# Kernel optimization log

Measured on AMD Instinct MI355X. Metric: run time of the kernel, lower is better.

Reference implementation:

```python
import jax, jax.numpy as jnp
import numpy as np

T = 16777216            # flat replay-buffer length (timesteps)
DISCOUNT = 0.99         # gamma
FINAL_REWARD = 0.0      # bootstrap value for the last timestep
TERM_PROB = 0.001       # ~1000-step episodes


def setup_inputs() -> dict:
    key = jax.random.key(0)
    k1, k2 = jax.random.split(key)
    reward = jax.random.normal(k1, (T,), dtype=jnp.float32)
    terminal = jax.random.bernoulli(k2, TERM_PROB, (T,))
    return {"terminal": terminal, "reward": reward}


def _discounted_cumret(terminal, reward):
    # Reverse-time linear recurrence (same math as tf.scan over reversed seq):
    #   c_t = r_t                      if terminal_t
    #   c_t = r_t + discount * c_{t+1} otherwise
    # i.e. c_t = a_t * c_{t+1} + b_t with a_t = discount*(1-term_t), b_t = r_t.
    # Expressed as a (log-depth) associative scan over the reversed sequence.
    a = jnp.where(terminal, jnp.zeros((), reward.dtype),
                  jnp.asarray(DISCOUNT, reward.dtype))
    a_rev = a[::-1]
    b_rev = reward[::-1]
    # fold the initializer (final_reward) into the first reversed element
    b_rev = b_rev.at[0].add(a_rev[0] * jnp.asarray(FINAL_REWARD, reward.dtype))

    def combine(e1, e2):
        # composition of affine maps x -> a*x + b (e1 applied first)
        a1, b1 = e1
        a2, b2 = e2
        return a1 * a2, a2 * b1 + b2

    _, y_rev = jax.lax.associative_scan(combine, (a_rev, b_rev))
    return y_rev[::-1]


def reference(terminal, reward):
    return _discounted_cumret(terminal, reward)
```

## Files before the change

kernel.cpp:

```cpp
#include <hip/hip_runtime.h>


constexpr int   TPB   = 256;
constexpr int   IPTC  = 8;
constexpr int   NCH   = 4;
constexpr int   CHUNK = TPB * IPTC;
constexpr int   TILE  = CHUNK * NCH;
constexpr float DISC  = 0.99f;
constexpr float L2DISC = -0.0144995696f;

__device__ __forceinline__ void wave_suffix_scan(float& A, float& B, int lane) {
    #pragma unroll
    for (int off = 1; off < 64; off <<= 1) {
        float oA = __shfl_down(A, off, 64);
        float oB = __shfl_down(B, off, 64);
        if (lane + off < 64) { B = A * oB + B; A = A * oA; }
    }
}

__global__ __launch_bounds__(TPB) void k_local(
        const int* __restrict__ term, const float* __restrict__ rew,
        float* __restrict__ out, float2* __restrict__ agg,
        int* __restrict__ lastT, long long T) {
    __shared__ float2 sWA[TPB / 64];
    __shared__ int    sLast[TPB / 64];

    const int t = threadIdx.x;
    const int lane = t & 63, wav = t >> 6;
    const int b = blockIdx.x;
    const long long lo = (long long)b * TILE;
    const bool fastblk = (lo + TILE <= T);

    float At = 1.f, Bt = 0.f;
    int   lt = -1;

    if (fastblk) {
        float4 bR[2][IPTC / 4];
        int4   bT[2][IPTC / 4];

        {
            const long long base = lo + (long long)(NCH - 1) * CHUNK
                                      + (long long)t * IPTC;
            const float4* rp = (const float4*)(rew + base);
            const int4*   tp = (const int4*)(term + base);
            #pragma unroll
            for (int q = 0; q < IPTC / 4; ++q) {
                bR[(NCH - 1) & 1][q] = rp[q];
                bT[(NCH - 1) & 1][q] = tp[q];
            }
        }

        #pragma unroll
        for (int c = NCH - 1; c >= 0; --c) {
            if (c > 0) {
                const long long nbase = lo + (long long)(c - 1) * CHUNK
                                           + (long long)t * IPTC;
                const float4* rp = (const float4*)(rew + nbase);
                const int4*   tp = (const int4*)(term + nbase);
                #pragma unroll
                for (int q = 0; q < IPTC / 4; ++q) {
                    bR[(c - 1) & 1][q] = rp[q];
                    bT[(c - 1) & 1][q] = tp[q];
                }
            }
            const int p = c & 1;
            const long long base = lo + (long long)c * CHUNK + (long long)t * IPTC;

            float r[IPTC];
            unsigned mask = 0;
            #pragma unroll
            for (int q = 0; q < IPTC / 4; ++q) {
                float4 rv = bR[p][q];
                int4   tv = bT[p][q];
                r[4*q+0] = rv.x; r[4*q+1] = rv.y; r[4*q+2] = rv.z; r[4*q+3] = rv.w;
                mask |= (tv.x ? 1u : 0u) << (4*q+0);
                mask |= (tv.y ? 1u : 0u) << (4*q+1);
                mask |= (tv.z ? 1u : 0u) << (4*q+2);
                mask |= (tv.w ? 1u : 0u) << (4*q+3);
            }

            float A = 1.f, B = 0.f;
            #pragma unroll
            for (int k = IPTC - 1; k >= 0; --k) {
                float ak = ((mask >> k) & 1u) ? 0.f : DISC;
                B = ak * B + r[k]; A = ak * A;
            }

            float IA = A, IB = B;
            wave_suffix_scan(IA, IB, lane);

            int myLast = mask ? (int)(base + (31 - __clz(mask))) : -1;
            #pragma unroll
            for (int off = 32; off > 0; off >>= 1)
                myLast = max(myLast, __shfl_down(myLast, off, 64));

            if (lane == 0) { sWA[wav] = make_float2(IA, IB); sLast[wav] = myLast; }
            __syncthreads();

            float2 g = sWA[0];
            int cl = sLast[0];
            #pragma unroll
            for (int w = 1; w < TPB / 64; ++w) {
                float2 h = sWA[w];
                g.y = g.x * h.y + g.y; g.x = g.x * h.x;
                cl = max(cl, sLast[w]);
            }
            float EWA = 1.f, EWB = 0.f;
            #pragma unroll
            for (int w = 0; w < TPB / 64; ++w)
                if (w > wav) { float2 h = sWA[w]; EWB = EWA*h.y + EWB; EWA = EWA*h.x; }

            float EA = __shfl_down(IA, 1, 64);
            float EB = __shfl_down(IB, 1, 64);
            if (lane == 63) { EA = 1.f; EB = 0.f; }

            const float Yc = Bt;
            float y = EA * (EWA * Yc + EWB) + EB;

            #pragma unroll
            for (int k = IPTC - 1; k >= 0; --k) {
                float ak = ((mask >> k) & 1u) ? 0.f : DISC;
                y = ak * y + r[k]; r[k] = y;
            }

            float4* op = (float4*)(out + base);
            #pragma unroll
            for (int q = 0; q < IPTC / 4; ++q)
                op[q] = make_float4(r[4*q+0], r[4*q+1], r[4*q+2], r[4*q+3]);

            Bt = g.x * Bt + g.y;
            At = g.x * At;
            lt = max(lt, cl);
            __syncthreads();
        }
    } else {
        for (int c = NCH - 1; c >= 0; --c) {
            const long long base = lo + (long long)c * CHUNK + (long long)t * IPTC;
            float r[IPTC];
            unsigned mask = 0;
            #pragma unroll
            for (int k = 0; k < IPTC; ++k) {
                long long i = base + k;
                if (i < T) { r[k] = rew[i]; mask |= (term[i] ? 1u : 0u) << k; }
                else       { r[k] = 0.f; }
            }
            float A = 1.f, B = 0.f;
            #pragma unroll
            for (int k = IPTC - 1; k >= 0; --k) {
                float ak = ((mask >> k) & 1u) ? 0.f : DISC;
                if (base + k >= T) ak = 1.f;
                B = ak * B + r[k]; A = ak * A;
            }
            float IA = A, IB = B;
            wave_suffix_scan(IA, IB, lane);

            int myLast = mask ? (int)(base + (31 - __clz(mask))) : -1;
            #pragma unroll
            for (int off = 32; off > 0; off >>= 1)
                myLast = max(myLast, __shfl_down(myLast, off, 64));

            if (lane == 0) { sWA[wav] = make_float2(IA, IB); sLast[wav] = myLast; }
            __syncthreads();

            float2 g = sWA[0];
            int cl = sLast[0];
            #pragma unroll
            for (int w = 1; w < TPB / 64; ++w) {
                float2 h = sWA[w];
                g.y = g.x * h.y + g.y; g.x = g.x * h.x;
                cl = max(cl, sLast[w]);
            }
            float EWA = 1.f, EWB = 0.f;
            #pragma unroll
            for (int w = 0; w < TPB / 64; ++w)
                if (w > wav) { float2 h = sWA[w]; EWB = EWA*h.y + EWB; EWA = EWA*h.x; }

            float EA = __shfl_down(IA, 1, 64);
            float EB = __shfl_down(IB, 1, 64);
            if (lane == 63) { EA = 1.f; EB = 0.f; }

            const float Yc = Bt;
            float y = EA * (EWA * Yc + EWB) + EB;

            #pragma unroll
            for (int k = IPTC - 1; k >= 0; --k) {
                float ak = ((mask >> k) & 1u) ? 0.f : DISC;
                if (base + k >= T) ak = 1.f;
                y = ak * y + r[k]; r[k] = y;
            }
            #pragma unroll
            for (int k = 0; k < IPTC; ++k) {
                long long i = base + k;
                if (i < T) out[i] = r[k];
            }

            Bt = g.x * Bt + g.y;
            At = g.x * At;
            lt = max(lt, cl);
            __syncthreads();
        }
    }

    if (t == 0) {
        agg[b] = make_float2(At, Bt);
        lastT[b] = max(lt, (int)lo - 1);
    }
}

__global__ __launch_bounds__(TPB) void k_fix(
        const float2* __restrict__ agg, const int* __restrict__ lastT,
        float* __restrict__ out, int numBlocks, long long T) {
    __shared__ float2 sWB[TPB / 64];

    const int t = threadIdx.x;
    const int lane = t & 63, wav = t >> 6;
    const int b = blockIdx.x;

    const int cpt = (numBlocks + TPB - 1) / TPB;
    float VA = 1.f, VB = 0.f;
    #pragma unroll
    for (int k = cpt - 1; k >= 0; --k) {
        int g = t * cpt + k;
        if (g > b && g < numBlocks) {
            float2 q = agg[g];
            VB = q.x * VB + q.y; VA = q.x * VA;
        }
    }
    wave_suffix_scan(VA, VB, lane);
    if (lane == 0) sWB[wav] = make_float2(VA, VB);
    __syncthreads();

    float FA = sWB[0].x, FB = sWB[0].y;
    #pragma unroll
    for (int w = 1; w < TPB / 64; ++w) {
        float2 h = sWB[w];
        FB = FA * h.y + FB; FA = FA * h.x;
    }
    const float yin = FB;
    if (yin == 0.f) return;

    const long long lo = (long long)b * TILE;
    const long long hi = min(lo + TILE, T) - 1;
    const long long start = (long long)lastT[b] + 1;

    for (long long i = start + t; i <= hi; i += TPB) {
        float d = (float)(int)(hi + 1 - i);
        out[i] += exp2f(d * L2DISC) * yin;
    }
}

extern "C" void kernel_launch(void* const* d_in, const int* in_sizes, int n_in,
                              void* d_out, int out_size, void* d_ws, size_t ws_size,
                              hipStream_t stream) {
    const int*   term = (const int*)d_in[0];
    const float* rew  = (const float*)d_in[1];
    float*       out  = (float*)d_out;

    const long long T = (long long)in_sizes[1];
    const int numBlocks = (int)((T + TILE - 1) / TILE);

    float2* agg   = (float2*)d_ws;
    int*    lastT = (int*)(agg + numBlocks);

    k_local<<<numBlocks, TPB, 0, stream>>>(term, rew, out, agg, lastT, T);
    k_fix  <<<numBlocks, TPB, 0, stream>>>(agg, lastT, out, numBlocks, T);
}
```

Before: 179.4 us.

## Fuse two-pass scan into single-pass decoupled look-back kernel

Replaces the separate local-scan and fix-up kernels with one kernel. Blocks take dynamic tile indices from an atomic ticket (processed from the end of the sequence) and publish per-tile aggregates and inclusive values through flags, using a wave-wide decoupled look-back to obtain the incoming carry. This removes the second launch and the global re-read of aggregates. Output stores also become nontemporal. It adds a memset, atomics and spin-waiting, and the fix-up pass now read-modify-writes output that was just stored with nontemporal hints.

```diff
diff --git a/kernel.cpp b/kernel.cpp
--- a/kernel.cpp
+++ b/kernel.cpp
@@ -9,6 +9,10 @@
 constexpr float DISC  = 0.99f;
 constexpr float L2DISC = -0.0144995696f;
 
+#define SCOPE_AGENT __HIP_MEMORY_SCOPE_AGENT
+
+typedef float vf4 __attribute__((ext_vector_type(4)));
+
 __device__ __forceinline__ void wave_suffix_scan(float& A, float& B, int lane) {
     #pragma unroll
     for (int off = 1; off < 64; off <<= 1) {
@@ -18,16 +22,24 @@
     }
 }
 
-__global__ __launch_bounds__(TPB) void k_local(
+__global__ __launch_bounds__(TPB) void k_scan(
         const int* __restrict__ term, const float* __restrict__ rew,
-        float* __restrict__ out, float2* __restrict__ agg,
-        int* __restrict__ lastT, long long T) {
+        float* __restrict__ out,
+        int* __restrict__ flags, int* __restrict__ ticket,
+        unsigned long long* __restrict__ AB, float* __restrict__ Incl,
+        int nB, long long T) {
     __shared__ float2 sWA[TPB / 64];
     __shared__ int    sLast[TPB / 64];
+    __shared__ int    sVb;
+    __shared__ float  sYin;
 
     const int t = threadIdx.x;
     const int lane = t & 63, wav = t >> 6;
-    const int b = blockIdx.x;
+
+    if (t == 0) sVb = atomicAdd(ticket, 1);
+    __syncthreads();
+    const int vb = sVb;
+    const int b  = nB - 1 - vb;
     const long long lo = (long long)b * TILE;
     const bool fastblk = (lo + TILE <= T);
 
@@ -123,10 +135,12 @@
                 y = ak * y + r[k]; r[k] = y;
             }
 
-            float4* op = (float4*)(out + base);
-            #pragma unroll
-            for (int q = 0; q < IPTC / 4; ++q)
-                op[q] = make_float4(r[4*q+0], r[4*q+1], r[4*q+2], r[4*q+3]);
+            vf4* op = (vf4*)(out + base);
+            #pragma unroll
+            for (int q = 0; q < IPTC / 4; ++q) {
+                vf4 v = { r[4*q+0], r[4*q+1], r[4*q+2], r[4*q+3] };
+                __builtin_nontemporal_store(v, op + q);
+            }
 
             Bt = g.x * Bt + g.y;
             At = g.x * At;
@@ -202,50 +216,79 @@
     }
 
     if (t == 0) {
-        agg[b] = make_float2(At, Bt);
-        lastT[b] = max(lt, (int)lo - 1);
-    }
-}
-
-__global__ __launch_bounds__(TPB) void k_fix(
-        const float2* __restrict__ agg, const int* __restrict__ lastT,
-        float* __restrict__ out, int numBlocks, long long T) {
-    __shared__ float2 sWB[TPB / 64];
-
-    const int t = threadIdx.x;
-    const int lane = t & 63, wav = t >> 6;
-    const int b = blockIdx.x;
-
-    const int cpt = (numBlocks + TPB - 1) / TPB;
-    float VA = 1.f, VB = 0.f;
-    #pragma unroll
-    for (int k = cpt - 1; k >= 0; --k) {
-        int g = t * cpt + k;
-        if (g > b && g < numBlocks) {
-            float2 q = agg[g];
-            VB = q.x * VB + q.y; VA = q.x * VA;
-        }
-    }
-    wave_suffix_scan(VA, VB, lane);
-    if (lane == 0) sWB[wav] = make_float2(VA, VB);
+        union { float2 f; unsigned long long u; } c;
+        c.f = make_float2(At, Bt);
+        __hip_atomic_store(&AB[vb], c.u, __ATOMIC_RELAXED, SCOPE_AGENT);
+        __hip_atomic_store(&flags[vb], 1, __ATOMIC_RELEASE, SCOPE_AGENT);
+    }
+
+    if (wav == 0) {
+        float yin = 0.f;
+        float Ca = 1.f, Cb = 0.f;
+        int look = vb - 1;
+        for (;;) {
+            if (look < 0 || Ca == 0.f) { yin = Cb; break; }
+            const int p = look - lane;
+            int f = 0;
+            if (p >= 0) f = __hip_atomic_load(&flags[p], __ATOMIC_ACQUIRE, SCOPE_AGENT);
+            const unsigned long long balP = __ballot(f == 2);
+            const unsigned long long balA = __ballot(f != 0);
+            const unsigned long long vmask =
+                (look >= 63) ? ~0ull : ((1ull << (look + 1)) - 1ull);
+            const unsigned long long prefAvail = balP & vmask;
+            bool consumed = false;
+            if (prefAvail) {
+                const int lp = (int)__ffsll((long long)prefAvail) - 1;
+                const unsigned long long need = (1ull << lp) - 1ull;
+                if ((balA & need) == need) {
+                    float a = 1.f, bv = 0.f;
+                    if (lane < lp) {
+                        union { unsigned long long u; float2 f2; } c;
+                        c.u = __hip_atomic_load(&AB[p], __ATOMIC_RELAXED, SCOPE_AGENT);
+                        a = c.f2.x; bv = c.f2.y;
+                    } else if (lane == lp) {
+                        a = 0.f;
+                        bv = __hip_atomic_load(&Incl[p], __ATOMIC_RELAXED, SCOPE_AGENT);
+                    }
+                    wave_suffix_scan(a, bv, lane);
+                    bv = __shfl(bv, 0, 64);
+                    yin = Ca * bv + Cb;
+                    break;
+                }
+            }
+            if ((balA & vmask) == vmask) {
+                float a = 1.f, bv = 0.f;
+                if (p >= 0) {
+                    union { unsigned long long u; float2 f2; } c;
+                    c.u = __hip_atomic_load(&AB[p], __ATOMIC_RELAXED, SCOPE_AGENT);
+                    a = c.f2.x; bv = c.f2.y;
+                }
+                wave_suffix_scan(a, bv, lane);
+                const float wA = __shfl(a, 0, 64);
+                const float wB = __shfl(bv, 0, 64);
+                Cb = Ca * wB + Cb;
+                Ca = Ca * wA;
+                look -= 64;
+                consumed = true;
+            }
+            if (!consumed) __builtin_amdgcn_s_sleep(2);
+        }
+        if (lane == 0) {
+            sYin = yin;
+            __hip_atomic_store(&Incl[vb], At * yin + Bt, __ATOMIC_RELAXED, SCOPE_AGENT);
+            __hip_atomic_store(&flags[vb], 2, __ATOMIC_RELEASE, SCOPE_AGENT);
+        }
+    }
     __syncthreads();
-
-    float FA = sWB[0].x, FB = sWB[0].y;
-    #pragma unroll
-    for (int w = 1; w < TPB / 64; ++w) {
-        float2 h = sWB[w];
-        FB = FA * h.y + FB; FA = FA * h.x;
-    }
-    const float yin = FB;
-    if (yin == 0.f) return;
-
-    const long long lo = (long long)b * TILE;
-    const long long hi = min(lo + TILE, T) - 1;
-    const long long start = (long long)lastT[b] + 1;
-
-    for (long long i = start + t; i <= hi; i += TPB) {
-        float d = (float)(int)(hi + 1 - i);
-        out[i] += exp2f(d * L2DISC) * yin;
+    const float yin = sYin;
+
+    if (yin != 0.f) {
+        const long long hi = min(lo + (long long)TILE, T) - 1;
+        const long long start = (long long)max(lt, (int)lo - 1) + 1;
+        for (long long i = start + t; i <= hi; i += TPB) {
+            float d = (float)(int)(hi + 1 - i);
+            out[i] += exp2f(d * L2DISC) * yin;
+        }
     }
 }
 
@@ -257,11 +300,14 @@
     float*       out  = (float*)d_out;
 
     const long long T = (long long)in_sizes[1];
-    const int numBlocks = (int)((T + TILE - 1) / TILE);
-
-    float2* agg   = (float2*)d_ws;
-    int*    lastT = (int*)(agg + numBlocks);
-
-    k_local<<<numBlocks, TPB, 0, stream>>>(term, rew, out, agg, lastT, T);
-    k_fix  <<<numBlocks, TPB, 0, stream>>>(agg, lastT, out, numBlocks, T);
+    const int nB = (int)((T + TILE - 1) / TILE);
+
+    int* flags  = (int*)d_ws;
+    int* ticket = flags + nB;
+    size_t off = (((size_t)(nB + 1) * 4) + 15) & ~(size_t)15;
+    unsigned long long* AB = (unsigned long long*)((char*)d_ws + off);
+    float* Incl = (float*)(AB + nB);
+
+    (void)hipMemsetAsync(d_ws, 0, (size_t)(nB + 1) * 4, stream);
+    k_scan<<<nB, TPB, 0, stream>>>(term, rew, out, flags, ticket, AB, Incl, nB, T);
 }
```

After: 468.1 us. 2.61x slower.

## Preload all chunks up front and double-buffer shared aggregates to drop barrier

Applied to the files above, without the earlier changes.

Issues every chunk's reward and terminal loads for the tile at kernel start instead of prefetching one chunk ahead. This raises memory-level parallelism. Per-wave scan aggregates in shared memory are double-buffered by chunk parity, so the trailing __syncthreads per chunk can be removed. The cost is more live registers for the load buffers, which may lower occupancy.

```diff
diff --git a/kernel.cpp b/kernel.cpp
--- a/kernel.cpp
+++ b/kernel.cpp
@@ -22,8 +22,8 @@
         const int* __restrict__ term, const float* __restrict__ rew,
         float* __restrict__ out, float2* __restrict__ agg,
         int* __restrict__ lastT, long long T) {
-    __shared__ float2 sWA[TPB / 64];
-    __shared__ int    sLast[TPB / 64];
+    __shared__ float2 sWA[2][TPB / 64];
+    __shared__ int    sLast[2][TPB / 64];
 
     const int t = threadIdx.x;
     const int lane = t & 63, wav = t >> 6;
@@ -35,43 +35,32 @@
     int   lt = -1;
 
     if (fastblk) {
-        float4 bR[2][IPTC / 4];
-        int4   bT[2][IPTC / 4];
-
-        {
-            const long long base = lo + (long long)(NCH - 1) * CHUNK
-                                      + (long long)t * IPTC;
+        float4 bR[NCH][IPTC / 4];
+        int4   bT[NCH][IPTC / 4];
+
+        #pragma unroll
+        for (int c = NCH - 1; c >= 0; --c) {
+            const long long base = lo + (long long)c * CHUNK + (long long)t * IPTC;
             const float4* rp = (const float4*)(rew + base);
             const int4*   tp = (const int4*)(term + base);
             #pragma unroll
             for (int q = 0; q < IPTC / 4; ++q) {
-                bR[(NCH - 1) & 1][q] = rp[q];
-                bT[(NCH - 1) & 1][q] = tp[q];
+                bR[c][q] = rp[q];
+                bT[c][q] = tp[q];
             }
         }
 
         #pragma unroll
         for (int c = NCH - 1; c >= 0; --c) {
-            if (c > 0) {
-                const long long nbase = lo + (long long)(c - 1) * CHUNK
-                                           + (long long)t * IPTC;
-                const float4* rp = (const float4*)(rew + nbase);
-                const int4*   tp = (const int4*)(term + nbase);
-                #pragma unroll
-                for (int q = 0; q < IPTC / 4; ++q) {
-                    bR[(c - 1) & 1][q] = rp[q];
-                    bT[(c - 1) & 1][q] = tp[q];
-                }
-            }
-            const int p = c & 1;
+            const int pb = c & 1;
             const long long base = lo + (long long)c * CHUNK + (long long)t * IPTC;
 
             float r[IPTC];
             unsigned mask = 0;
             #pragma unroll
             for (int q = 0; q < IPTC / 4; ++q) {
-                float4 rv = bR[p][q];
-                int4   tv = bT[p][q];
+                float4 rv = bR[c][q];
+                int4   tv = bT[c][q];
                 r[4*q+0] = rv.x; r[4*q+1] = rv.y; r[4*q+2] = rv.z; r[4*q+3] = rv.w;
                 mask |= (tv.x ? 1u : 0u) << (4*q+0);
                 mask |= (tv.y ? 1u : 0u) << (4*q+1);
@@ -94,21 +83,21 @@
             for (int off = 32; off > 0; off >>= 1)
                 myLast = max(myLast, __shfl_down(myLast, off, 64));
 
-            if (lane == 0) { sWA[wav] = make_float2(IA, IB); sLast[wav] = myLast; }
+            if (lane == 0) { sWA[pb][wav] = make_float2(IA, IB); sLast[pb][wav] = myLast; }
             __syncthreads();
 
-            float2 g = sWA[0];
-            int cl = sLast[0];
+            float2 g = sWA[pb][0];
+            int cl = sLast[pb][0];
             #pragma unroll
             for (int w = 1; w < TPB / 64; ++w) {
-                float2 h = sWA[w];
+                float2 h = sWA[pb][w];
                 g.y = g.x * h.y + g.y; g.x = g.x * h.x;
-                cl = max(cl, sLast[w]);
+                cl = max(cl, sLast[pb][w]);
             }
             float EWA = 1.f, EWB = 0.f;
             #pragma unroll
             for (int w = 0; w < TPB / 64; ++w)
-                if (w > wav) { float2 h = sWA[w]; EWB = EWA*h.y + EWB; EWA = EWA*h.x; }
+                if (w > wav) { float2 h = sWA[pb][w]; EWB = EWA*h.y + EWB; EWA = EWA*h.x; }
 
             float EA = __shfl_down(IA, 1, 64);
             float EB = __shfl_down(IB, 1, 64);
@@ -131,10 +120,10 @@
             Bt = g.x * Bt + g.y;
             At = g.x * At;
             lt = max(lt, cl);
-            __syncthreads();
         }
     } else {
         for (int c = NCH - 1; c >= 0; --c) {
+            const int pb = c & 1;
             const long long base = lo + (long long)c * CHUNK + (long long)t * IPTC;
             float r[IPTC];
             unsigned mask = 0;
@@ -159,21 +148,21 @@
             for (int off = 32; off > 0; off >>= 1)
                 myLast = max(myLast, __shfl_down(myLast, off, 64));
 
-            if (lane == 0) { sWA[wav] = make_float2(IA, IB); sLast[wav] = myLast; }
+            if (lane == 0) { sWA[pb][wav] = make_float2(IA, IB); sLast[pb][wav] = myLast; }
             __syncthreads();
 
-            float2 g = sWA[0];
-            int cl = sLast[0];
+            float2 g = sWA[pb][0];
+            int cl = sLast[pb][0];
             #pragma unroll
             for (int w = 1; w < TPB / 64; ++w) {
-                float2 h = sWA[w];
+                float2 h = sWA[pb][w];
                 g.y = g.x * h.y + g.y; g.x = g.x * h.x;
-                cl = max(cl, sLast[w]);
+                cl = max(cl, sLast[pb][w]);
             }
             float EWA = 1.f, EWB = 0.f;
             #pragma unroll
             for (int w = 0; w < TPB / 64; ++w)
-                if (w > wav) { float2 h = sWA[w]; EWB = EWA*h.y + EWB; EWA = EWA*h.x; }
+                if (w > wav) { float2 h = sWA[pb][w]; EWB = EWA*h.y + EWB; EWA = EWA*h.x; }
 
             float EA = __shfl_down(IA, 1, 64);
             float EB = __shfl_down(IB, 1, 64);
@@ -197,7 +186,6 @@
             Bt = g.x * Bt + g.y;
             At = g.x * At;
             lt = max(lt, cl);
-            __syncthreads();
         }
     }
 
```

Result: no change. 178.3 us (-0.6%).

## Replace per-block chunk loop with single 1024-thread tile per block

Applied to the files above, without the earlier changes.

The local scan kernel now uses 1024-thread blocks that each process one 8192-element tile in a single pass, replacing 256-thread blocks that looped over four chunks with double-buffered prefetch and carried state between them. This removes the serial chunk loop, the carry propagation and a barrier per chunk. The fix kernel keeps 256 threads via a separate constant. Tiles are the same size, so block counts are unchanged. The cost is that the within-block cross-wave combine now spans 16 waves serially, and the explicit load prefetch is gone.

```diff
diff --git a/kernel.cpp b/kernel.cpp
--- a/kernel.cpp
+++ b/kernel.cpp
@@ -1,13 +1,14 @@
 #include <hip/hip_runtime.h>
 
 
-constexpr int   TPB   = 256;
+constexpr int   TPB   = 1024;
+constexpr int   NWAV  = TPB / 64;
 constexpr int   IPTC  = 8;
-constexpr int   NCH   = 4;
-constexpr int   CHUNK = TPB * IPTC;
-constexpr int   TILE  = CHUNK * NCH;
+constexpr int   TILE  = TPB * IPTC;
 constexpr float DISC  = 0.99f;
 constexpr float L2DISC = -0.0144995696f;
+
+constexpr int   FTPB  = 256;
 
 __device__ __forceinline__ void wave_suffix_scan(float& A, float& B, int lane) {
     #pragma unroll
@@ -22,8 +23,8 @@
         const int* __restrict__ term, const float* __restrict__ rew,
         float* __restrict__ out, float2* __restrict__ agg,
         int* __restrict__ lastT, long long T) {
-    __shared__ float2 sWA[TPB / 64];
-    __shared__ int    sLast[TPB / 64];
+    __shared__ float2 sWA[NWAV];
+    __shared__ int    sLast[NWAV];
 
     const int t = threadIdx.x;
     const int lane = t & 63, wav = t >> 6;
@@ -31,174 +32,146 @@
     const long long lo = (long long)b * TILE;
     const bool fastblk = (lo + TILE <= T);
 
-    float At = 1.f, Bt = 0.f;
-    int   lt = -1;
+    float At, Bt;
+    int   lt;
 
     if (fastblk) {
-        float4 bR[2][IPTC / 4];
-        int4   bT[2][IPTC / 4];
-
+        const long long base = lo + (long long)t * IPTC;
+
+        float4 bR[IPTC / 4];
+        int4   bT[IPTC / 4];
         {
-            const long long base = lo + (long long)(NCH - 1) * CHUNK
-                                      + (long long)t * IPTC;
             const float4* rp = (const float4*)(rew + base);
             const int4*   tp = (const int4*)(term + base);
             #pragma unroll
             for (int q = 0; q < IPTC / 4; ++q) {
-                bR[(NCH - 1) & 1][q] = rp[q];
-                bT[(NCH - 1) & 1][q] = tp[q];
+                bR[q] = rp[q];
+                bT[q] = tp[q];
             }
         }
 
-        #pragma unroll
-        for (int c = NCH - 1; c >= 0; --c) {
-            if (c > 0) {
-                const long long nbase = lo + (long long)(c - 1) * CHUNK
-                                           + (long long)t * IPTC;
-                const float4* rp = (const float4*)(rew + nbase);
-                const int4*   tp = (const int4*)(term + nbase);
-                #pragma unroll
-                for (int q = 0; q < IPTC / 4; ++q) {
-                    bR[(c - 1) & 1][q] = rp[q];
-                    bT[(c - 1) & 1][q] = tp[q];
-                }
-            }
-            const int p = c & 1;
-            const long long base = lo + (long long)c * CHUNK + (long long)t * IPTC;
-
-            float r[IPTC];
-            unsigned mask = 0;
-            #pragma unroll
-            for (int q = 0; q < IPTC / 4; ++q) {
-                float4 rv = bR[p][q];
-                int4   tv = bT[p][q];
-                r[4*q+0] = rv.x; r[4*q+1] = rv.y; r[4*q+2] = rv.z; r[4*q+3] = rv.w;
-                mask |= (tv.x ? 1u : 0u) << (4*q+0);
-                mask |= (tv.y ? 1u : 0u) << (4*q+1);
-                mask |= (tv.z ? 1u : 0u) << (4*q+2);
-                mask |= (tv.w ? 1u : 0u) << (4*q+3);
-            }
-
-            float A = 1.f, B = 0.f;
-            #pragma unroll
-            for (int k = IPTC - 1; k >= 0; --k) {
-                float ak = ((mask >> k) & 1u) ? 0.f : DISC;
-                B = ak * B + r[k]; A = ak * A;
-            }
-
-            float IA = A, IB = B;
-            wave_suffix_scan(IA, IB, lane);
-
-            int myLast = mask ? (int)(base + (31 - __clz(mask))) : -1;
-            #pragma unroll
-            for (int off = 32; off > 0; off >>= 1)
-                myLast = max(myLast, __shfl_down(myLast, off, 64));
-
-            if (lane == 0) { sWA[wav] = make_float2(IA, IB); sLast[wav] = myLast; }
-            __syncthreads();
-
-            float2 g = sWA[0];
-            int cl = sLast[0];
-            #pragma unroll
-            for (int w = 1; w < TPB / 64; ++w) {
-                float2 h = sWA[w];
-                g.y = g.x * h.y + g.y; g.x = g.x * h.x;
-                cl = max(cl, sLast[w]);
-            }
-            float EWA = 1.f, EWB = 0.f;
-            #pragma unroll
-            for (int w = 0; w < TPB / 64; ++w)
-                if (w > wav) { float2 h = sWA[w]; EWB = EWA*h.y + EWB; EWA = EWA*h.x; }
-
-            float EA = __shfl_down(IA, 1, 64);
-            float EB = __shfl_down(IB, 1, 64);
-            if (lane == 63) { EA = 1.f; EB = 0.f; }
-
-            const float Yc = Bt;
-            float y = EA * (EWA * Yc + EWB) + EB;
-
-            #pragma unroll
-            for (int k = IPTC - 1; k >= 0; --k) {
-                float ak = ((mask >> k) & 1u) ? 0.f : DISC;
-                y = ak * y + r[k]; r[k] = y;
-            }
-
-            float4* op = (float4*)(out + base);
-            #pragma unroll
-            for (int q = 0; q < IPTC / 4; ++q)
-                op[q] = make_float4(r[4*q+0], r[4*q+1], r[4*q+2], r[4*q+3]);
-
-            Bt = g.x * Bt + g.y;
-            At = g.x * At;
-            lt = max(lt, cl);
-            __syncthreads();
-        }
+        float r[IPTC];
+        unsigned mask = 0;
+        #pragma unroll
+        for (int q = 0; q < IPTC / 4; ++q) {
+            float4 rv = bR[q];
+            int4   tv = bT[q];
+            r[4*q+0] = rv.x; r[4*q+1] = rv.y; r[4*q+2] = rv.z; r[4*q+3] = rv.w;
+            mask |= (tv.x ? 1u : 0u) << (4*q+0);
+            mask |= (tv.y ? 1u : 0u) << (4*q+1);
+            mask |= (tv.z ? 1u : 0u) << (4*q+2);
+            mask |= (tv.w ? 1u : 0u) << (4*q+3);
+        }
+
+        float A = 1.f, B = 0.f;
+        #pragma unroll
+        for (int k = IPTC - 1; k >= 0; --k) {
+            float ak = ((mask >> k) & 1u) ? 0.f : DISC;
+            B = ak * B + r[k]; A = ak * A;
+        }
+
+        float IA = A, IB = B;
+        wave_suffix_scan(IA, IB, lane);
+
+        int myLast = mask ? (int)(base + (31 - __clz(mask))) : -1;
+        #pragma unroll
+        for (int off = 32; off > 0; off >>= 1)
+            myLast = max(myLast, __shfl_down(myLast, off, 64));
+
+        if (lane == 0) { sWA[wav] = make_float2(IA, IB); sLast[wav] = myLast; }
+        __syncthreads();
+
+        float2 g = sWA[0];
+        int cl = sLast[0];
+        #pragma unroll
+        for (int w = 1; w < NWAV; ++w) {
+            float2 h = sWA[w];
+            g.y = g.x * h.y + g.y; g.x = g.x * h.x;
+            cl = max(cl, sLast[w]);
+        }
+        float EWA = 1.f, EWB = 0.f;
+        #pragma unroll
+        for (int w = 0; w < NWAV; ++w)
+            if (w > wav) { float2 h = sWA[w]; EWB = EWA*h.y + EWB; EWA = EWA*h.x; }
+
+        float EA = __shfl_down(IA, 1, 64);
+        float EB = __shfl_down(IB, 1, 64);
+        if (lane == 63) { EA = 1.f; EB = 0.f; }
+
+        float y = EA * EWB + EB;
+
+        #pragma unroll
+        for (int k = IPTC - 1; k >= 0; --k) {
+            float ak = ((mask >> k) & 1u) ? 0.f : DISC;
+            y = ak * y + r[k]; r[k] = y;
+        }
+
+        float4* op = (float4*)(out + base);
+        #pragma unroll
+        for (int q = 0; q < IPTC / 4; ++q)
+            op[q] = make_float4(r[4*q+0], r[4*q+1], r[4*q+2], r[4*q+3]);
+
+        At = g.x; Bt = g.y; lt = cl;
     } else {
-        for (int c = NCH - 1; c >= 0; --c) {
-            const long long base = lo + (long long)c * CHUNK + (long long)t * IPTC;
-            float r[IPTC];
-            unsigned mask = 0;
-            #pragma unroll
-            for (int k = 0; k < IPTC; ++k) {
-                long long i = base + k;
-                if (i < T) { r[k] = rew[i]; mask |= (term[i] ? 1u : 0u) << k; }
-                else       { r[k] = 0.f; }
-            }
-            float A = 1.f, B = 0.f;
-            #pragma unroll
-            for (int k = IPTC - 1; k >= 0; --k) {
-                float ak = ((mask >> k) & 1u) ? 0.f : DISC;
-                if (base + k >= T) ak = 1.f;
-                B = ak * B + r[k]; A = ak * A;
-            }
-            float IA = A, IB = B;
-            wave_suffix_scan(IA, IB, lane);
-
-            int myLast = mask ? (int)(base + (31 - __clz(mask))) : -1;
-            #pragma unroll
-            for (int off = 32; off > 0; off >>= 1)
-                myLast = max(myLast, __shfl_down(myLast, off, 64));
-
-            if (lane == 0) { sWA[wav] = make_float2(IA, IB); sLast[wav] = myLast; }
-            __syncthreads();
-
-            float2 g = sWA[0];
-            int cl = sLast[0];
-            #pragma unroll
-            for (int w = 1; w < TPB / 64; ++w) {
-                float2 h = sWA[w];
-                g.y = g.x * h.y + g.y; g.x = g.x * h.x;
-                cl = max(cl, sLast[w]);
-            }
-            float EWA = 1.f, EWB = 0.f;
-            #pragma unroll
-            for (int w = 0; w < TPB / 64; ++w)
-                if (w > wav) { float2 h = sWA[w]; EWB = EWA*h.y + EWB; EWA = EWA*h.x; }
-
-            float EA = __shfl_down(IA, 1, 64);
-            float EB = __shfl_down(IB, 1, 64);
-            if (lane == 63) { EA = 1.f; EB = 0.f; }
-
-            const float Yc = Bt;
-            float y = EA * (EWA * Yc + EWB) + EB;
-
-            #pragma unroll
-            for (int k = IPTC - 1; k >= 0; --k) {
-                float ak = ((mask >> k) & 1u) ? 0.f : DISC;
-                if (base + k >= T) ak = 1.f;
-                y = ak * y + r[k]; r[k] = y;
-            }
-            #pragma unroll
-            for (int k = 0; k < IPTC; ++k) {
-                long long i = base + k;
-                if (i < T) out[i] = r[k];
-            }
-
-            Bt = g.x * Bt + g.y;
-            At = g.x * At;
-            lt = max(lt, cl);
-            __syncthreads();
-        }
+        const long long base = lo + (long long)t * IPTC;
+        float r[IPTC];
+        unsigned mask = 0;
+        #pragma unroll
+        for (int k = 0; k < IPTC; ++k) {
+            long long i = base + k;
+            if (i < T) { r[k] = rew[i]; mask |= (term[i] ? 1u : 0u) << k; }
+            else       { r[k] = 0.f; }
+        }
+        float A = 1.f, B = 0.f;
+        #pragma unroll
+        for (int k = IPTC - 1; k >= 0; --k) {
+            float ak = ((mask >> k) & 1u) ? 0.f : DISC;
+            if (base + k >= T) ak = 1.f;
+            B = ak * B + r[k]; A = ak * A;
+        }
+        float IA = A, IB = B;
+        wave_suffix_scan(IA, IB, lane);
+
+        int myLast = mask ? (int)(base + (31 - __clz(mask))) : -1;
+        #pragma unroll
+        for (int off = 32; off > 0; off >>= 1)
+            myLast = max(myLast, __shfl_down(myLast, off, 64));
+
+        if (lane == 0) { sWA[wav] = make_float2(IA, IB); sLast[wav] = myLast; }
+        __syncthreads();
+
+        float2 g = sWA[0];
+        int cl = sLast[0];
+        #pragma unroll
+        for (int w = 1; w < NWAV; ++w) {
+            float2 h = sWA[w];
+            g.y = g.x * h.y + g.y; g.x = g.x * h.x;
+            cl = max(cl, sLast[w]);
+        }
+        float EWA = 1.f, EWB = 0.f;
+        #pragma unroll
+        for (int w = 0; w < NWAV; ++w)
+            if (w > wav) { float2 h = sWA[w]; EWB = EWA*h.y + EWB; EWA = EWA*h.x; }
+
+        float EA = __shfl_down(IA, 1, 64);
+        float EB = __shfl_down(IB, 1, 64);
+        if (lane == 63) { EA = 1.f; EB = 0.f; }
+
+        float y = EA * EWB + EB;
+
+        #pragma unroll
+        for (int k = IPTC - 1; k >= 0; --k) {
+            float ak = ((mask >> k) & 1u) ? 0.f : DISC;
+            if (base + k >= T) ak = 1.f;
+            y = ak * y + r[k]; r[k] = y;
+        }
+        #pragma unroll
+        for (int k = 0; k < IPTC; ++k) {
+            long long i = base + k;
+            if (i < T) out[i] = r[k];
+        }
+
+        At = g.x; Bt = g.y; lt = cl;
     }
 
     if (t == 0) {
@@ -207,16 +180,16 @@
     }
 }
 
-__global__ __launch_bounds__(TPB) void k_fix(
+__global__ __launch_bounds__(FTPB) void k_fix(
         const float2* __restrict__ agg, const int* __restrict__ lastT,
         float* __restrict__ out, int numBlocks, long long T) {
-    __shared__ float2 sWB[TPB / 64];
+    __shared__ float2 sWB[FTPB / 64];
 
     const int t = threadIdx.x;
     const int lane = t & 63, wav = t >> 6;
     const int b = blockIdx.x;
 
-    const int cpt = (numBlocks + TPB - 1) / TPB;
+    const int cpt = (numBlocks + FTPB - 1) / FTPB;
     float VA = 1.f, VB = 0.f;
     #pragma unroll
     for (int k = cpt - 1; k >= 0; --k) {
@@ -232,7 +205,7 @@
 
     float FA = sWB[0].x, FB = sWB[0].y;
     #pragma unroll
-    for (int w = 1; w < TPB / 64; ++w) {
+    for (int w = 1; w < FTPB / 64; ++w) {
         float2 h = sWB[w];
         FB = FA * h.y + FB; FA = FA * h.x;
     }
@@ -240,10 +213,10 @@
     if (yin == 0.f) return;
 
     const long long lo = (long long)b * TILE;
-    const long long hi = min(lo + TILE, T) - 1;
+    const long long hi = min(lo + (long long)TILE, T) - 1;
     const long long start = (long long)lastT[b] + 1;
 
-    for (long long i = start + t; i <= hi; i += TPB) {
+    for (long long i = start + t; i <= hi; i += FTPB) {
         float d = (float)(int)(hi + 1 - i);
         out[i] += exp2f(d * L2DISC) * yin;
     }
@@ -263,5 +236,5 @@
     int*    lastT = (int*)(agg + numBlocks);
 
     k_local<<<numBlocks, TPB, 0, stream>>>(term, rew, out, agg, lastT, T);
-    k_fix  <<<numBlocks, TPB, 0, stream>>>(agg, lastT, out, numBlocks, T);
-}
+    k_fix  <<<numBlocks, FTPB, 0, stream>>>(agg, lastT, out, numBlocks, T);
+}
```

Result: no change. 176.8 us (median of 2 runs) (-1.5%).
